# Performance work log

Hardware: AMD Instinct MI355X
Metric: run time of the kernel (lower is better)

Reference implementation:

```python
import jax, jax.numpy as jnp
import numpy as np

B, T, V, H = 1024, 256, 256, 32
SIGMA = 0.01


def setup_inputs() -> dict:
    key = jax.random.key(0)
    k0, k1, k2, k3 = jax.random.split(key, 4)
    X = jax.random.randint(k0, (B, T), 0, V)  # token ids [batch, num_steps]
    W_xh = jax.random.normal(k1, (V, H), dtype=jnp.float32) * SIGMA
    W_hh = jax.random.normal(k2, (H, H), dtype=jnp.float32) * SIGMA
    b_h = jnp.zeros((H,), dtype=jnp.float32)
    W_hq = jax.random.normal(k3, (H, V), dtype=jnp.float32) * SIGMA
    b_q = jnp.zeros((V,), dtype=jnp.float32)
    return {"X": X, "W_xh": W_xh, "W_hh": W_hh, "b_h": b_h, "W_hq": W_hq, "b_q": b_q}


def reference(X, W_xh, W_hh, b_h, W_hq, b_q):
    # one_hot(X.T, V) @ W_xh  ==  row-gather of W_xh  -> [T, B, H] (time-major)
    x_emb = W_xh[X.T]
    h0 = jnp.zeros((X.shape[0], W_hh.shape[0]), dtype=W_hh.dtype)  # [B, H]

    def step(h, xe):
        h = jnp.tanh(xe + h @ W_hh + b_h)
        return h, h

    _, hs = jax.lax.scan(step, h0, x_emb)  # hs: [T, B, H]
    # output layer, stacked on axis 1 as in the torch code -> [B, T, V]
    logits = jnp.einsum('tbh,hv->btv', hs, W_hq) + b_q
    return logits
```

## Files before the change

kernel.cpp:

```cpp
#include <hip/hip_runtime.h>


#define B_SZ 1024
#define T_SZ 256
#define V_SZ 256
#define H_SZ 32
#define HP   40
#define NCH  16
#define CS   16

typedef _Float16 f16x8 __attribute__((ext_vector_type(8)));
typedef float    f32x4 __attribute__((ext_vector_type(4)));

__device__ __forceinline__ float lane_bcast(float v, int lane) {
    return __int_as_float(__builtin_amdgcn_readlane(__float_as_int(v), lane));
}

__device__ __forceinline__ float fast_tanh(float x) {
    float z = __expf(2.0f * x);
    return (z - 1.0f) * __builtin_amdgcn_rcpf(z + 1.0f);
}

__global__ __launch_bounds__(256, 1) void rnnlm_fused(
    const int*   __restrict__ X,
    const float* __restrict__ W_xh,
    const float* __restrict__ W_hh,
    const float* __restrict__ b_h,
    const float* __restrict__ W_hq,
    const float* __restrict__ b_q,
    float*       __restrict__ out)
{
    __shared__ __align__(16) _Float16 s_whqT[V_SZ][H_SZ];
    __shared__ __align__(16) _Float16 s_hist[4][2][CS][HP];

    const int tid   = threadIdx.x;
    const int wv    = tid >> 6;
    const int lane  = tid & 63;
    const int l15   = lane & 15;
    const int kg    = lane >> 4;
    const int batch = blockIdx.x * 4 + wv;

    #pragma unroll
    for (int k = 0; k < H_SZ; ++k)
        s_whqT[tid][k] = (_Float16)W_hq[k * V_SZ + tid];
    __syncthreads();

    f16x8 aw[16];
    f32x4 bq4[16];
    #pragma unroll
    for (int vt = 0; vt < 16; ++vt) {
        aw[vt]  = *(const f16x8*)&s_whqT[vt * 16 + l15][kg * 8];
        bq4[vt] = *(const f32x4*)(b_q + vt * 16 + 4 * kg);
    }

    float whh[H_SZ];
    float bh = 0.0f, h = 0.0f;
    float e0 = 0.0f, e1 = 0.0f, e2 = 0.0f;
    int   tkA = 0, tkB = 0, tkC = 0;
    const int* Xr = X + batch * T_SZ;
    if (lane < H_SZ) {
        #pragma unroll
        for (int i = 0; i < H_SZ; ++i)
            whh[i] = W_hh[i * H_SZ + lane];
        bh  = b_h[lane];
        tkA = Xr[3]; tkB = Xr[4]; tkC = Xr[5];
        e0 = W_xh[Xr[0] * H_SZ + lane];
        e1 = W_xh[Xr[1] * H_SZ + lane];
        e2 = W_xh[Xr[2] * H_SZ + lane];
    }

    float* outb = out + (size_t)batch * T_SZ * V_SZ;

    for (int c = 0; c < NCH; ++c) {
        const int buf = c & 1;

        if (lane < H_SZ) {
            for (int s = 0; s < CS; ++s) {
                const int t = c * CS + s;
                float a0 = e0 + bh, a1 = 0.0f, a2 = 0.0f, a3 = 0.0f;
                e0 = e1; e1 = e2;
                e2 = W_xh[tkA * H_SZ + lane];
                tkA = tkB; tkB = tkC;
                tkC = Xr[t + 6 < T_SZ ? t + 6 : T_SZ - 1];

                #pragma unroll
                for (int i = 0; i < H_SZ; i += 4) {
                    a0 += lane_bcast(h, i + 0) * whh[i + 0];
                    a1 += lane_bcast(h, i + 1) * whh[i + 1];
                    a2 += lane_bcast(h, i + 2) * whh[i + 2];
                    a3 += lane_bcast(h, i + 3) * whh[i + 3];
                }
                h = fast_tanh((a0 + a1) + (a2 + a3));
                s_hist[wv][buf][s][lane] = (_Float16)h;
            }
        }
        asm volatile("" ::: "memory");

        const f16x8 hfrag = *(const f16x8*)&s_hist[wv][buf][l15][kg * 8];

        float* p = outb + ((size_t)(c * CS + l15)) * V_SZ + 4 * kg;
        #pragma unroll
        for (int vt = 0; vt < 16; ++vt) {
            f32x4 acc = bq4[vt];
            acc = __builtin_amdgcn_mfma_f32_16x16x32_f16(aw[vt], hfrag, acc,
                                                         0, 0, 0);
            *(f32x4*)(p + vt * 16) = acc;
        }
    }
}

extern "C" void kernel_launch(void* const* d_in, const int* in_sizes, int n_in,
                              void* d_out, int out_size, void* d_ws, size_t ws_size,
                              hipStream_t stream) {
    const int*   X    = (const int*)d_in[0];
    const float* W_xh = (const float*)d_in[1];
    const float* W_hh = (const float*)d_in[2];
    const float* b_h  = (const float*)d_in[3];
    const float* W_hq = (const float*)d_in[4];
    const float* b_q  = (const float*)d_in[5];
    float* out = (float*)d_out;

    rnnlm_fused<<<dim3(B_SZ / 4), dim3(256), 0, stream>>>(X, W_xh, W_hh, b_h,
                                                          W_hq, b_q, out);
}
```

Measured before the change: 304.9 us.

## Split RNN into producer and consumer waves with double-buffered history

Doubles the block to 512 threads. Four producer waves run the serial tanh recurrence for the next chunk while four consumer waves run the MFMA output projection and store the previous chunk, exchanging data through a double-buffered shared-memory history with a block barrier per chunk. The aim is to overlap the latency-bound recurrence with the store-heavy output stage. It adds a barrier per chunk, and each wave may get fewer resources now that there are twice as many waves per block.

```diff
diff --git a/kernel.cpp b/kernel.cpp
--- a/kernel.cpp
+++ b/kernel.cpp
@@ -21,7 +21,7 @@
     return (z - 1.0f) * __builtin_amdgcn_rcpf(z + 1.0f);
 }
 
-__global__ __launch_bounds__(256, 1) void rnnlm_fused(
+__global__ __launch_bounds__(512, 1) void rnnlm_fused(
     const int*   __restrict__ X,
     const float* __restrict__ W_xh,
     const float* __restrict__ W_hh,
@@ -33,56 +33,50 @@
     __shared__ __align__(16) _Float16 s_whqT[V_SZ][H_SZ];
     __shared__ __align__(16) _Float16 s_hist[4][2][CS][HP];
 
-    const int tid   = threadIdx.x;
-    const int wv    = tid >> 6;
-    const int lane  = tid & 63;
-    const int l15   = lane & 15;
-    const int kg    = lane >> 4;
-    const int batch = blockIdx.x * 4 + wv;
+    const int tid  = threadIdx.x;
+    const int wvid = tid >> 6;
+    const int lane = tid & 63;
+    const int l15  = lane & 15;
+    const int kg   = lane >> 4;
+    const bool producer = (wvid < 4);
+    const int pb = wvid & 3;
+    const int batch = blockIdx.x * 4 + pb;
 
-    #pragma unroll
-    for (int k = 0; k < H_SZ; ++k)
-        s_whqT[tid][k] = (_Float16)W_hq[k * V_SZ + tid];
+    if (tid < V_SZ) {
+        #pragma unroll
+        for (int k = 0; k < H_SZ; ++k)
+            s_whqT[tid][k] = (_Float16)W_hq[k * V_SZ + tid];
+    }
     __syncthreads();
-
-    f16x8 aw[16];
-    f32x4 bq4[16];
-    #pragma unroll
-    for (int vt = 0; vt < 16; ++vt) {
-        aw[vt]  = *(const f16x8*)&s_whqT[vt * 16 + l15][kg * 8];
-        bq4[vt] = *(const f32x4*)(b_q + vt * 16 + 4 * kg);
-    }
 
     float whh[H_SZ];
     float bh = 0.0f, h = 0.0f;
     float e0 = 0.0f, e1 = 0.0f, e2 = 0.0f;
     int   tkA = 0, tkB = 0, tkC = 0;
     const int* Xr = X + batch * T_SZ;
-    if (lane < H_SZ) {
-        #pragma unroll
-        for (int i = 0; i < H_SZ; ++i)
-            whh[i] = W_hh[i * H_SZ + lane];
-        bh  = b_h[lane];
-        tkA = Xr[3]; tkB = Xr[4]; tkC = Xr[5];
-        e0 = W_xh[Xr[0] * H_SZ + lane];
-        e1 = W_xh[Xr[1] * H_SZ + lane];
-        e2 = W_xh[Xr[2] * H_SZ + lane];
-    }
-
+    f16x8 aw[16];
+    f32x4 bq4[16];
     float* outb = out + (size_t)batch * T_SZ * V_SZ;
 
-    for (int c = 0; c < NCH; ++c) {
-        const int buf = c & 1;
-
+    if (producer) {
+        if (lane < H_SZ) {
+            #pragma unroll
+            for (int i = 0; i < H_SZ; ++i)
+                whh[i] = W_hh[i * H_SZ + lane];
+            bh  = b_h[lane];
+            tkA = Xr[3]; tkB = Xr[4]; tkC = Xr[5];
+            e0 = W_xh[Xr[0] * H_SZ + lane];
+            e1 = W_xh[Xr[1] * H_SZ + lane];
+            e2 = W_xh[Xr[2] * H_SZ + lane];
+        }
         if (lane < H_SZ) {
             for (int s = 0; s < CS; ++s) {
-                const int t = c * CS + s;
+                const int t = s;
                 float a0 = e0 + bh, a1 = 0.0f, a2 = 0.0f, a3 = 0.0f;
                 e0 = e1; e1 = e2;
                 e2 = W_xh[tkA * H_SZ + lane];
                 tkA = tkB; tkB = tkC;
                 tkC = Xr[t + 6 < T_SZ ? t + 6 : T_SZ - 1];
-
                 #pragma unroll
                 for (int i = 0; i < H_SZ; i += 4) {
                     a0 += lane_bcast(h, i + 0) * whh[i + 0];
@@ -91,21 +85,53 @@
                     a3 += lane_bcast(h, i + 3) * whh[i + 3];
                 }
                 h = fast_tanh((a0 + a1) + (a2 + a3));
-                s_hist[wv][buf][s][lane] = (_Float16)h;
+                s_hist[pb][0][s][lane] = (_Float16)h;
             }
         }
-        asm volatile("" ::: "memory");
-
-        const f16x8 hfrag = *(const f16x8*)&s_hist[wv][buf][l15][kg * 8];
-
-        float* p = outb + ((size_t)(c * CS + l15)) * V_SZ + 4 * kg;
+    } else {
         #pragma unroll
         for (int vt = 0; vt < 16; ++vt) {
-            f32x4 acc = bq4[vt];
-            acc = __builtin_amdgcn_mfma_f32_16x16x32_f16(aw[vt], hfrag, acc,
-                                                         0, 0, 0);
-            *(f32x4*)(p + vt * 16) = acc;
+            aw[vt]  = *(const f16x8*)&s_whqT[vt * 16 + l15][kg * 8];
+            bq4[vt] = *(const f32x4*)(b_q + vt * 16 + 4 * kg);
         }
+    }
+    __syncthreads();
+
+    for (int c = 0; c < NCH; ++c) {
+        if (producer) {
+            if (c + 1 < NCH && lane < H_SZ) {
+                const int cc = c + 1, buf = cc & 1;
+                for (int s = 0; s < CS; ++s) {
+                    const int t = cc * CS + s;
+                    float a0 = e0 + bh, a1 = 0.0f, a2 = 0.0f, a3 = 0.0f;
+                    e0 = e1; e1 = e2;
+                    e2 = W_xh[tkA * H_SZ + lane];
+                    tkA = tkB; tkB = tkC;
+                    tkC = Xr[t + 6 < T_SZ ? t + 6 : T_SZ - 1];
+                    #pragma unroll
+                    for (int i = 0; i < H_SZ; i += 4) {
+                        a0 += lane_bcast(h, i + 0) * whh[i + 0];
+                        a1 += lane_bcast(h, i + 1) * whh[i + 1];
+                        a2 += lane_bcast(h, i + 2) * whh[i + 2];
+                        a3 += lane_bcast(h, i + 3) * whh[i + 3];
+                    }
+                    h = fast_tanh((a0 + a1) + (a2 + a3));
+                    s_hist[pb][buf][s][lane] = (_Float16)h;
+                }
+            }
+        } else {
+            const int buf = c & 1;
+            const f16x8 hfrag = *(const f16x8*)&s_hist[pb][buf][l15][kg * 8];
+            float* p = outb + ((size_t)(c * CS + l15)) * V_SZ + 4 * kg;
+            #pragma unroll
+            for (int vt = 0; vt < 16; ++vt) {
+                f32x4 acc = bq4[vt];
+                acc = __builtin_amdgcn_mfma_f32_16x16x32_f16(aw[vt], hfrag,
+                                                             acc, 0, 0, 0);
+                *(f32x4*)(p + vt * 16) = acc;
+            }
+        }
+        __syncthreads();
     }
 }
 
@@ -120,6 +146,6 @@
     const float* b_q  = (const float*)d_in[5];
     float* out = (float*)d_out;
 
-    rnnlm_fused<<<dim3(B_SZ / 4), dim3(256), 0, stream>>>(X, W_xh, W_hh, b_h,
+    rnnlm_fused<<<dim3(B_SZ / 4), dim3(512), 0, stream>>>(X, W_xh, W_hh, b_h,
                                                           W_hq, b_q, out);
 }
```

Result: faster. 291.1 us (-4.5%).
